# Kernel optimization log

Measured on AMD Instinct MI355X. Metric: run time of the kernel, lower is better.

Reference implementation:

```python
import jax, jax.numpy as jnp
import numpy as np

RES, GATE, SKIP, K, DIL, CIN = 128, 256, 128, 3, 2, 80
PAD = (K - 1) * DIL


def _wn(v, g):
    # weight_norm: w = g * v / ||v||, norm over all dims except dim 0 (out_channels)
    norm = jnp.sqrt(jnp.sum(v * v, axis=(1, 2), keepdims=True))
    return v * (g.reshape(-1, 1, 1) / norm)


def setup_inputs() -> dict:
    key = jax.random.key(0)
    ks = jax.random.split(key, 12)
    s = lambda *sh: 1.0 / np.sqrt(np.prod(sh[1:]))
    d = {
        "x": jax.random.normal(ks[0], (8, RES, 32768), dtype=jnp.float32),
        "condition": jax.random.normal(ks[1], (8, CIN, 32768), dtype=jnp.float32),
        "conv_v": jax.random.normal(ks[2], (GATE, RES, K), dtype=jnp.float32) * s(GATE, RES, K),
        "conv_g": jnp.ones((GATE,), dtype=jnp.float32),
        "conv_b": jnp.zeros((GATE,), dtype=jnp.float32),
        "lc_v": jax.random.normal(ks[3], (GATE, CIN, 1), dtype=jnp.float32) * s(GATE, CIN, 1),
        "lc_g": jnp.ones((GATE,), dtype=jnp.float32),
        "skip_v": jax.random.normal(ks[4], (SKIP, GATE // 2, 1), dtype=jnp.float32) * s(SKIP, GATE // 2, 1),
        "skip_g": jnp.ones((SKIP,), dtype=jnp.float32),
        "skip_b": jnp.zeros((SKIP,), dtype=jnp.float32),
        "out_v": jax.random.normal(ks[5], (RES, GATE // 2, 1), dtype=jnp.float32) * s(RES, GATE // 2, 1),
        "out_g": jnp.ones((RES,), dtype=jnp.float32),
        "out_b": jnp.zeros((RES,), dtype=jnp.float32),
    }
    return d


def reference(x, condition, conv_v, conv_g, conv_b, lc_v, lc_g,
              skip_v, skip_g, skip_b, out_v, out_g, out_b):
    residual = x
    w = _wn(conv_v, conv_g)  # [GATE, RES, K]
    # torch pads symmetrically then slices [:, :, :-PAD]; equivalent to left-only pad
    h = jax.lax.conv_general_dilated(
        x, w, window_strides=(1,), padding=[(PAD, 0)], rhs_dilation=(DIL,),
        dimension_numbers=("NCH", "OIH", "NCH"))
    h = h + conv_b[None, :, None]  # [B, GATE, T]
    a, b = jnp.split(h, 2, axis=1)
    lc_w = _wn(lc_v, lc_g)[:, :, 0]  # [GATE, CIN]
    c = jnp.einsum("oc,bct->bot", lc_w, condition)
    ca, cb = jnp.split(c, 2, axis=1)
    g = jnp.tanh(a + ca) * jax.nn.sigmoid(b + cb)  # [B, GATE//2, T]
    skip_w = _wn(skip_v, skip_g)[:, :, 0]
    s = jnp.einsum("oc,bct->bot", skip_w, g) + skip_b[None, :, None]
    out_w = _wn(out_v, out_g)[:, :, 0]
    o = jnp.einsum("oc,bct->bot", out_w, g) + out_b[None, :, None]
    return (o + residual, s)
```

## Files before the change

kernel.cpp:

```cpp
#include <hip/hip_runtime.h>
#include <hip/hip_bf16.h>

#define B_N   8
#define T_N   32768
#define RESC  128
#define GATEC 256
#define CINC  80
#define CINP  96
#define NT    64
#define HALO  4
#define XROWS 68
#define XSTR  136
#define CSTR  96
#define HSTR  136

#define AP1_ELEMS (16*12*512)
#define AP2_ELEMS (16*3*512)
#define AP3_ELEMS (16*4*512)

#define OFF_S ((size_t)B_N * RESC * T_N)

typedef __attribute__((ext_vector_type(8))) short short8;
typedef __attribute__((ext_vector_type(4))) float f32x4;

__device__ __forceinline__ ushort f2bf(float f) {
  union { float f; unsigned int u; } c; c.f = f;
  unsigned int u = c.u;
  u += 0x7fffu + ((u >> 16) & 1u);
  return (ushort)(u >> 16);
}
__device__ __forceinline__ float bf2f(ushort s) {
  union { unsigned int u; float f; } c; c.u = ((unsigned int)s) << 16;
  return c.f;
}

__global__ __launch_bounds__(256) void wn_pack_kernel(
    const float* __restrict__ conv_v, const float* __restrict__ conv_g,
    const float* __restrict__ lc_v,  const float* __restrict__ lc_g,
    const float* __restrict__ skip_v,const float* __restrict__ skip_g,
    const float* __restrict__ out_v, const float* __restrict__ out_g,
    ushort* __restrict__ Ap1, ushort* __restrict__ Ap2, ushort* __restrict__ Ap3) {
  const int o   = blockIdx.x;
  const int tid = threadIdx.x;
  const int mtg = o >> 4, r = o & 15;
  __shared__ float red[256];

  float s = 0.f;
  for (int e = tid; e < RESC * 3; e += 256) { float v = conv_v[o * RESC * 3 + e]; s += v * v; }
  red[tid] = s; __syncthreads();
  for (int off = 128; off > 0; off >>= 1) { if (tid < off) red[tid] += red[tid + off]; __syncthreads(); }
  const float csc = conv_g[o] / sqrtf(red[0]);
  __syncthreads();
  for (int e = tid; e < 384; e += 256) {
    const int ks = e >> 5, q = (e >> 3) & 3, j = e & 7;
    const int tap = ks >> 2, ci = (ks & 3) * 32 + q * 8 + j;
    Ap1[((mtg * 12 + ks) * 64 + q * 16 + r) * 8 + j] = f2bf(conv_v[(o * RESC + ci) * 3 + tap] * csc);
  }

  s = 0.f;
  for (int e = tid; e < CINC; e += 256) { float v = lc_v[o * CINC + e]; s += v * v; }
  red[tid] = s; __syncthreads();
  for (int off = 128; off > 0; off >>= 1) { if (tid < off) red[tid] += red[tid + off]; __syncthreads(); }
  const float lsc = lc_g[o] / sqrtf(red[0]);
  __syncthreads();
  for (int e = tid; e < CINP; e += 256) {
    const int ks = e >> 5, q = (e >> 3) & 3, j = e & 7;
    const float wv = (e < CINC) ? lc_v[o * CINC + e] * lsc : 0.f;
    Ap2[((mtg * 3 + ks) * 64 + q * 16 + r) * 8 + j] = f2bf(wv);
  }

  const float* vrow = (o < 128) ? (skip_v + o * 128) : (out_v + (o - 128) * 128);
  const float  gg   = (o < 128) ? skip_g[o] : out_g[o - 128];
  s = 0.f;
  for (int e = tid; e < 128; e += 256) { float v = vrow[e]; s += v * v; }
  red[tid] = s; __syncthreads();
  for (int off = 128; off > 0; off >>= 1) { if (tid < off) red[tid] += red[tid + off]; __syncthreads(); }
  const float ssc = gg / sqrtf(red[0]);
  for (int e = tid; e < 128; e += 256) {
    const int ks = e >> 5, q = (e >> 3) & 3, j = e & 7;
    Ap3[((mtg * 4 + ks) * 64 + q * 16 + r) * 8 + j] = f2bf(vrow[e] * ssc);
  }
}

__global__ __launch_bounds__(256) void fused_block_kernel(
    const float* __restrict__ x, const float* __restrict__ cond,
    const float* __restrict__ conv_b, const float* __restrict__ skip_b,
    const float* __restrict__ out_b,
    const ushort* __restrict__ Ap1, const ushort* __restrict__ Ap2,
    const ushort* __restrict__ Ap3,
    float* __restrict__ out) {
  const int tid  = threadIdx.x;
  const int w    = tid >> 6;
  const int lane = tid & 63;
  const int q    = lane >> 4;
  const int n    = lane & 15;
  const int blk  = blockIdx.x;
  const int b    = blk >> 9;
  const int t0   = (blk & 511) << 6;

  __shared__ ushort smem[17408];
  ushort* xs  = smem;
  ushort* cs  = smem + XROWS * XSTR;
  ushort* hsA = smem;
  ushort* hsB = smem + NT * HSTR;

  {
    const int g4 = tid >> 3;
    const int c0 = g4 << 2;
    const int tt = (tid & 7) << 3;
    const float* xp = x + ((size_t)b * RESC + c0) * T_N + t0 + tt;
    float va[4][8];
#pragma unroll
    for (int rr = 0; rr < 4; ++rr) {
      const float4* rp = (const float4*)(xp + (size_t)rr * T_N);
      const float4 a0 = rp[0], a1 = rp[1];
      va[rr][0] = a0.x; va[rr][1] = a0.y; va[rr][2] = a0.z; va[rr][3] = a0.w;
      va[rr][4] = a1.x; va[rr][5] = a1.y; va[rr][6] = a1.z; va[rr][7] = a1.w;
    }
#pragma unroll
    for (int ss = 0; ss < 8; ++ss) {
      const unsigned lo = (unsigned)f2bf(va[0][ss]) | ((unsigned)f2bf(va[1][ss]) << 16);
      const unsigned hi = (unsigned)f2bf(va[2][ss]) | ((unsigned)f2bf(va[3][ss]) << 16);
      *(uint2*)&xs[(HALO + tt + ss) * XSTR + c0] = make_uint2(lo, hi);
    }
  }
  if (tid < RESC) {
    float h0 = 0.f, h1 = 0.f, h2 = 0.f, h3 = 0.f;
    if (t0 > 0) {
      const float4 hv = *(const float4*)(x + ((size_t)b * RESC + tid) * T_N + t0 - 4);
      h0 = hv.x; h1 = hv.y; h2 = hv.z; h3 = hv.w;
    }
    xs[0 * XSTR + tid] = f2bf(h0);
    xs[1 * XSTR + tid] = f2bf(h1);
    xs[2 * XSTR + tid] = f2bf(h2);
    xs[3 * XSTR + tid] = f2bf(h3);
  }
  if (tid < 160) {
    const int g4 = tid >> 3;
    const int c0 = g4 << 2;
    const int tt = (tid & 7) << 3;
    const float* cp = cond + ((size_t)b * CINC + c0) * T_N + t0 + tt;
    float va[4][8];
#pragma unroll
    for (int rr = 0; rr < 4; ++rr) {
      const float4* rp = (const float4*)(cp + (size_t)rr * T_N);
      const float4 a0 = rp[0], a1 = rp[1];
      va[rr][0] = a0.x; va[rr][1] = a0.y; va[rr][2] = a0.z; va[rr][3] = a0.w;
      va[rr][4] = a1.x; va[rr][5] = a1.y; va[rr][6] = a1.z; va[rr][7] = a1.w;
    }
#pragma unroll
    for (int ss = 0; ss < 8; ++ss) {
      const unsigned lo = (unsigned)f2bf(va[0][ss]) | ((unsigned)f2bf(va[1][ss]) << 16);
      const unsigned hi = (unsigned)f2bf(va[2][ss]) | ((unsigned)f2bf(va[3][ss]) << 16);
      *(uint2*)&cs[(tt + ss) * CSTR + c0] = make_uint2(lo, hi);
    }
  } else {
    const int e0 = tid - 160;
    for (int z = e0; z < 512; z += 96) {
      const int t = z >> 3, cp2 = z & 7;
      *(unsigned int*)&cs[t * CSTR + CINC + cp2 * 2] = 0u;
    }
  }
  __syncthreads();

  f32x4 acc[4][4];
#pragma unroll
  for (int mt = 0; mt < 4; ++mt) {
    const float4 cb = *(const float4*)(conv_b + w * 64 + mt * 16 + q * 4);
#pragma unroll
    for (int nt = 0; nt < 4; ++nt) acc[mt][nt] = (f32x4){cb.x, cb.y, cb.z, cb.w};
  }
#pragma unroll
  for (int ks = 0; ks < 12; ++ks) {
    const int tap = ks >> 2;
    const int cb2 = (ks & 3) << 5;
    short8 af[4], bfr[4];
#pragma unroll
    for (int mt = 0; mt < 4; ++mt)
      af[mt] = *(const short8*)(Ap1 + ((w * 4 + mt) * 12 + ks) * 512 + lane * 8);
#pragma unroll
    for (int nt = 0; nt < 4; ++nt)
      bfr[nt] = *(const short8*)&xs[(nt * 16 + n + tap * 2) * XSTR + cb2 + q * 8];
#pragma unroll
    for (int mt = 0; mt < 4; ++mt)
#pragma unroll
      for (int nt = 0; nt < 4; ++nt)
        acc[mt][nt] = __builtin_amdgcn_mfma_f32_16x16x32_bf16(af[mt], bfr[nt], acc[mt][nt], 0, 0, 0);
  }
#pragma unroll
  for (int ks = 0; ks < 3; ++ks) {
    short8 af[4], bfr[4];
#pragma unroll
    for (int mt = 0; mt < 4; ++mt)
      af[mt] = *(const short8*)(Ap2 + ((w * 4 + mt) * 3 + ks) * 512 + lane * 8);
#pragma unroll
    for (int nt = 0; nt < 4; ++nt)
      bfr[nt] = *(const short8*)&cs[(nt * 16 + n) * CSTR + ks * 32 + q * 8];
#pragma unroll
    for (int mt = 0; mt < 4; ++mt)
#pragma unroll
      for (int nt = 0; nt < 4; ++nt)
        acc[mt][nt] = __builtin_amdgcn_mfma_f32_16x16x32_bf16(af[mt], bfr[nt], acc[mt][nt], 0, 0, 0);
  }
  __syncthreads();

  const int colbase = (w & 1) << 6;
  {
    ushort* hdst = (w < 2) ? hsA : hsB;
#pragma unroll
    for (int mt = 0; mt < 4; ++mt)
#pragma unroll
      for (int nt = 0; nt < 4; ++nt) {
        const f32x4 v = acc[mt][nt];
        float r0, r1, r2, r3;
        if (w < 2) {
          r0 = 1.f - 2.f / (__expf(2.f * v[0]) + 1.f);
          r1 = 1.f - 2.f / (__expf(2.f * v[1]) + 1.f);
          r2 = 1.f - 2.f / (__expf(2.f * v[2]) + 1.f);
          r3 = 1.f - 2.f / (__expf(2.f * v[3]) + 1.f);
        } else {
          r0 = 1.f / (1.f + __expf(-v[0]));
          r1 = 1.f / (1.f + __expf(-v[1]));
          r2 = 1.f / (1.f + __expf(-v[2]));
          r3 = 1.f / (1.f + __expf(-v[3]));
        }
        const unsigned lo = (unsigned)f2bf(r0) | ((unsigned)f2bf(r1) << 16);
        const unsigned hi = (unsigned)f2bf(r2) | ((unsigned)f2bf(r3) << 16);
        *(uint2*)&hdst[(nt * 16 + n) * HSTR + colbase + mt * 16 + q * 4] = make_uint2(lo, hi);
      }
  }
  __syncthreads();

  {
    const int prow = tid >> 2;
    const int pc0  = (tid & 3) << 5;
#pragma unroll
    for (int s2 = 0; s2 < 8; ++s2) {
      const int col = pc0 + (s2 << 2);
      const uint2 ua = *(uint2*)&hsA[prow * HSTR + col];
      const uint2 ub = *(uint2*)&hsB[prow * HSTR + col];
      const float a0 = bf2f((ushort)ua.x), a1 = bf2f((ushort)(ua.x >> 16));
      const float a2 = bf2f((ushort)ua.y), a3 = bf2f((ushort)(ua.y >> 16));
      const float b0 = bf2f((ushort)ub.x), b1 = bf2f((ushort)(ub.x >> 16));
      const float b2 = bf2f((ushort)ub.y), b3 = bf2f((ushort)(ub.y >> 16));
      const unsigned lo = (unsigned)f2bf(a0 * b0) | ((unsigned)f2bf(a1 * b1) << 16);
      const unsigned hi = (unsigned)f2bf(a2 * b2) | ((unsigned)f2bf(a3 * b3) << 16);
      *(uint2*)&hsA[prow * HSTR + col] = make_uint2(lo, hi);
    }
  }
  __syncthreads();

  {
    const float* bias = (w < 2) ? skip_b : out_b;
#pragma unroll
    for (int mt = 0; mt < 4; ++mt) {
      const float4 bb = *(const float4*)(bias + colbase + mt * 16 + q * 4);
#pragma unroll
      for (int nt = 0; nt < 4; ++nt) acc[mt][nt] = (f32x4){bb.x, bb.y, bb.z, bb.w};
    }
#pragma unroll
    for (int ks = 0; ks < 4; ++ks) {
      short8 af[4], bfr[4];
#pragma unroll
      for (int mt = 0; mt < 4; ++mt)
        af[mt] = *(const short8*)(Ap3 + ((w * 4 + mt) * 4 + ks) * 512 + lane * 8);
#pragma unroll
      for (int nt = 0; nt < 4; ++nt)
        bfr[nt] = *(const short8*)&hsA[(nt * 16 + n) * HSTR + ks * 32 + q * 8];
#pragma unroll
      for (int mt = 0; mt < 4; ++mt)
#pragma unroll
        for (int nt = 0; nt < 4; ++nt)
          acc[mt][nt] = __builtin_amdgcn_mfma_f32_16x16x32_bf16(af[mt], bfr[nt], acc[mt][nt], 0, 0, 0);
    }
  }

#pragma unroll
  for (int mt = 0; mt < 4; ++mt)
#pragma unroll
    for (int nt = 0; nt < 4; ++nt) {
      const int ch = colbase + mt * 16 + q * 4;
      const int t  = t0 + nt * 16 + n;
      const f32x4 v = acc[mt][nt];
      if (w < 2) {
        float* dst = out + OFF_S + ((size_t)(b * RESC + ch)) * T_N + t;
#pragma unroll
        for (int i = 0; i < 4; ++i) dst[(size_t)i * T_N] = v[i];
      } else {
        const float* xr = x + ((size_t)(b * RESC + ch)) * T_N + t;
        float* dst = out + ((size_t)(b * RESC + ch)) * T_N + t;
#pragma unroll
        for (int i = 0; i < 4; ++i) dst[(size_t)i * T_N] = v[i] + xr[(size_t)i * T_N];
      }
    }
}

extern "C" void kernel_launch(void* const* d_in, const int* in_sizes, int n_in,
                              void* d_out, int out_size, void* d_ws, size_t ws_size,
                              hipStream_t stream) {
  const float* x      = (const float*)d_in[0];
  const float* cond   = (const float*)d_in[1];
  const float* conv_v = (const float*)d_in[2];
  const float* conv_g = (const float*)d_in[3];
  const float* conv_b = (const float*)d_in[4];
  const float* lc_v   = (const float*)d_in[5];
  const float* lc_g   = (const float*)d_in[6];
  const float* skip_v = (const float*)d_in[7];
  const float* skip_g = (const float*)d_in[8];
  const float* skip_b = (const float*)d_in[9];
  const float* out_v  = (const float*)d_in[10];
  const float* out_g  = (const float*)d_in[11];
  const float* out_b  = (const float*)d_in[12];

  ushort* Ap1 = (ushort*)d_ws;
  ushort* Ap2 = Ap1 + AP1_ELEMS;
  ushort* Ap3 = Ap2 + AP2_ELEMS;

  hipLaunchKernelGGL(wn_pack_kernel, dim3(256), dim3(256), 0, stream,
                     conv_v, conv_g, lc_v, lc_g, skip_v, skip_g, out_v, out_g,
                     Ap1, Ap2, Ap3);
  hipLaunchKernelGGL(fused_block_kernel, dim3(4096), dim3(256), 0, stream,
                     x, cond, conv_b, skip_b, out_b, Ap1, Ap2, Ap3, (float*)d_out);
}
```

Baseline: 511.5 us.

## Fuse gating in registers by pairing tanh/sigmoid tiles per wave, swizzle LDS

Each wave now owns matching tanh and sigmoid output tiles (rows 2w,2w+1 and 8+2w,9+2w). The gate product can then be computed in registers, which removes the separate LDS round trip, one bf16 rounding step and one barrier. LDS rows use an XOR swizzle in place of padded strides, and the LDS footprint shrinks. A launch-bounds occupancy hint of 5 blocks per CU is added, which may constrain registers and cause spills.

New measurement: 965.5 us. 1.89x slower.

```diff
diff --git a/kernel.cpp b/kernel.cpp
--- a/kernel.cpp
+++ b/kernel.cpp
@@ -1,5 +1,4 @@
 #include <hip/hip_runtime.h>
-#include <hip/hip_bf16.h>
 
 #define B_N   8
 #define T_N   32768
@@ -10,9 +9,11 @@
 #define NT    64
 #define HALO  4
 #define XROWS 68
-#define XSTR  136
-#define CSTR  96
-#define HSTR  136
+
+#define XSTR_B 272
+#define CSTR_B 208
+#define CS_OFF 18496
+#define LDS_BYTES (18496 + 13312)
 
 #define AP1_ELEMS (16*12*512)
 #define AP2_ELEMS (16*3*512)
@@ -29,9 +30,11 @@
   u += 0x7fffu + ((u >> 16) & 1u);
   return (ushort)(u >> 16);
 }
-__device__ __forceinline__ float bf2f(ushort s) {
-  union { unsigned int u; float f; } c; c.u = ((unsigned int)s) << 16;
-  return c.f;
+
+__device__ __forceinline__ char* lds_at(char* base, int row, int strB, int colB) {
+  int off = row * strB + colB;
+  off ^= ((row >> 3) & 7) << 4;
+  return base + off;
 }
 
 __global__ __launch_bounds__(256) void wn_pack_kernel(
@@ -82,7 +85,7 @@
   }
 }
 
-__global__ __launch_bounds__(256) void fused_block_kernel(
+__global__ __launch_bounds__(256, 5) void fused_block_kernel(
     const float* __restrict__ x, const float* __restrict__ cond,
     const float* __restrict__ conv_b, const float* __restrict__ skip_b,
     const float* __restrict__ out_b,
@@ -98,11 +101,10 @@
   const int b    = blk >> 9;
   const int t0   = (blk & 511) << 6;
 
-  __shared__ ushort smem[17408];
-  ushort* xs  = smem;
-  ushort* cs  = smem + XROWS * XSTR;
-  ushort* hsA = smem;
-  ushort* hsB = smem + NT * HSTR;
+  __shared__ __align__(128) char smem[LDS_BYTES];
+  char* xs = smem;
+  char* cs = smem + CS_OFF;
+  char* gs = smem;
 
   {
     const int g4 = tid >> 3;
@@ -121,7 +123,7 @@
     for (int ss = 0; ss < 8; ++ss) {
       const unsigned lo = (unsigned)f2bf(va[0][ss]) | ((unsigned)f2bf(va[1][ss]) << 16);
       const unsigned hi = (unsigned)f2bf(va[2][ss]) | ((unsigned)f2bf(va[3][ss]) << 16);
-      *(uint2*)&xs[(HALO + tt + ss) * XSTR + c0] = make_uint2(lo, hi);
+      *(uint2*)lds_at(xs, HALO + tt + ss, XSTR_B, c0 * 2) = make_uint2(lo, hi);
     }
   }
   if (tid < RESC) {
@@ -130,10 +132,10 @@
       const float4 hv = *(const float4*)(x + ((size_t)b * RESC + tid) * T_N + t0 - 4);
       h0 = hv.x; h1 = hv.y; h2 = hv.z; h3 = hv.w;
     }
-    xs[0 * XSTR + tid] = f2bf(h0);
-    xs[1 * XSTR + tid] = f2bf(h1);
-    xs[2 * XSTR + tid] = f2bf(h2);
-    xs[3 * XSTR + tid] = f2bf(h3);
+    *(ushort*)lds_at(xs, 0, XSTR_B, tid * 2) = f2bf(h0);
+    *(ushort*)lds_at(xs, 1, XSTR_B, tid * 2) = f2bf(h1);
+    *(ushort*)lds_at(xs, 2, XSTR_B, tid * 2) = f2bf(h2);
+    *(ushort*)lds_at(xs, 3, XSTR_B, tid * 2) = f2bf(h3);
   }
   if (tid < 160) {
     const int g4 = tid >> 3;
@@ -152,35 +154,36 @@
     for (int ss = 0; ss < 8; ++ss) {
       const unsigned lo = (unsigned)f2bf(va[0][ss]) | ((unsigned)f2bf(va[1][ss]) << 16);
       const unsigned hi = (unsigned)f2bf(va[2][ss]) | ((unsigned)f2bf(va[3][ss]) << 16);
-      *(uint2*)&cs[(tt + ss) * CSTR + c0] = make_uint2(lo, hi);
+      *(uint2*)lds_at(cs, tt + ss, CSTR_B, c0 * 2) = make_uint2(lo, hi);
     }
   } else {
     const int e0 = tid - 160;
     for (int z = e0; z < 512; z += 96) {
-      const int t = z >> 3, cp2 = z & 7;
-      *(unsigned int*)&cs[t * CSTR + CINC + cp2 * 2] = 0u;
-    }
-  }
-  __syncthreads();
-
+      const int row = z >> 3, c = z & 7;
+      *(unsigned int*)lds_at(cs, row, CSTR_B, 160 + c * 4) = 0u;
+    }
+  }
+  __syncthreads();
+
+  const int mtile[4] = {2 * w, 2 * w + 1, 8 + 2 * w, 9 + 2 * w};
   f32x4 acc[4][4];
 #pragma unroll
   for (int mt = 0; mt < 4; ++mt) {
-    const float4 cb = *(const float4*)(conv_b + w * 64 + mt * 16 + q * 4);
+    const float4 cb = *(const float4*)(conv_b + mtile[mt] * 16 + q * 4);
 #pragma unroll
     for (int nt = 0; nt < 4; ++nt) acc[mt][nt] = (f32x4){cb.x, cb.y, cb.z, cb.w};
   }
 #pragma unroll
   for (int ks = 0; ks < 12; ++ks) {
     const int tap = ks >> 2;
-    const int cb2 = (ks & 3) << 5;
+    const int cbyte = ((ks & 3) << 6);
     short8 af[4], bfr[4];
 #pragma unroll
     for (int mt = 0; mt < 4; ++mt)
-      af[mt] = *(const short8*)(Ap1 + ((w * 4 + mt) * 12 + ks) * 512 + lane * 8);
+      af[mt] = *(const short8*)(Ap1 + ((mtile[mt] * 12 + ks) * 64 + lane) * 8);
 #pragma unroll
     for (int nt = 0; nt < 4; ++nt)
-      bfr[nt] = *(const short8*)&xs[(nt * 16 + n + tap * 2) * XSTR + cb2 + q * 8];
+      bfr[nt] = *(const short8*)lds_at(xs, nt * 16 + n + tap * 2, XSTR_B, cbyte + q * 16);
 #pragma unroll
     for (int mt = 0; mt < 4; ++mt)
 #pragma unroll
@@ -192,10 +195,10 @@
     short8 af[4], bfr[4];
 #pragma unroll
     for (int mt = 0; mt < 4; ++mt)
-      af[mt] = *(const short8*)(Ap2 + ((w * 4 + mt) * 3 + ks) * 512 + lane * 8);
+      af[mt] = *(const short8*)(Ap2 + ((mtile[mt] * 3 + ks) * 64 + lane) * 8);
 #pragma unroll
     for (int nt = 0; nt < 4; ++nt)
-      bfr[nt] = *(const short8*)&cs[(nt * 16 + n) * CSTR + ks * 32 + q * 8];
+      bfr[nt] = *(const short8*)lds_at(cs, nt * 16 + n, CSTR_B, ks * 64 + q * 16);
 #pragma unroll
     for (int mt = 0; mt < 4; ++mt)
 #pragma unroll
@@ -204,53 +207,27 @@
   }
   __syncthreads();
 
+#pragma unroll
+  for (int mt = 0; mt < 2; ++mt)
+#pragma unroll
+    for (int nt = 0; nt < 4; ++nt) {
+      const f32x4 va = acc[mt][nt];
+      const f32x4 vb = acc[mt + 2][nt];
+      float r[4];
+#pragma unroll
+      for (int i = 0; i < 4; ++i) {
+        const float ta = 1.f - 2.f / (__expf(2.f * va[i]) + 1.f);
+        const float sb = 1.f / (1.f + __expf(-vb[i]));
+        r[i] = ta * sb;
+      }
+      const unsigned lo = (unsigned)f2bf(r[0]) | ((unsigned)f2bf(r[1]) << 16);
+      const unsigned hi = (unsigned)f2bf(r[2]) | ((unsigned)f2bf(r[3]) << 16);
+      *(uint2*)lds_at(gs, nt * 16 + n, XSTR_B, 64 * w + 32 * mt + 8 * q) = make_uint2(lo, hi);
+    }
+  __syncthreads();
+
   const int colbase = (w & 1) << 6;
   {
-    ushort* hdst = (w < 2) ? hsA : hsB;
-#pragma unroll
-    for (int mt = 0; mt < 4; ++mt)
-#pragma unroll
-      for (int nt = 0; nt < 4; ++nt) {
-        const f32x4 v = acc[mt][nt];
-        float r0, r1, r2, r3;
-        if (w < 2) {
-          r0 = 1.f - 2.f / (__expf(2.f * v[0]) + 1.f);
-          r1 = 1.f - 2.f / (__expf(2.f * v[1]) + 1.f);
-          r2 = 1.f - 2.f / (__expf(2.f * v[2]) + 1.f);
-          r3 = 1.f - 2.f / (__expf(2.f * v[3]) + 1.f);
-        } else {
-          r0 = 1.f / (1.f + __expf(-v[0]));
-          r1 = 1.f / (1.f + __expf(-v[1]));
-          r2 = 1.f / (1.f + __expf(-v[2]));
-          r3 = 1.f / (1.f + __expf(-v[3]));
-        }
-        const unsigned lo = (unsigned)f2bf(r0) | ((unsigned)f2bf(r1) << 16);
-        const unsigned hi = (unsigned)f2bf(r2) | ((unsigned)f2bf(r3) << 16);
-        *(uint2*)&hdst[(nt * 16 + n) * HSTR + colbase + mt * 16 + q * 4] = make_uint2(lo, hi);
-      }
-  }
-  __syncthreads();
-
-  {
-    const int prow = tid >> 2;
-    const int pc0  = (tid & 3) << 5;
-#pragma unroll
-    for (int s2 = 0; s2 < 8; ++s2) {
-      const int col = pc0 + (s2 << 2);
-      const uint2 ua = *(uint2*)&hsA[prow * HSTR + col];
-      const uint2 ub = *(uint2*)&hsB[prow * HSTR + col];
-      const float a0 = bf2f((ushort)ua.x), a1 = bf2f((ushort)(ua.x >> 16));
-      const float a2 = bf2f((ushort)ua.y), a3 = bf2f((ushort)(ua.y >> 16));
-      const float b0 = bf2f((ushort)ub.x), b1 = bf2f((ushort)(ub.x >> 16));
-      const float b2 = bf2f((ushort)ub.y), b3 = bf2f((ushort)(ub.y >> 16));
-      const unsigned lo = (unsigned)f2bf(a0 * b0) | ((unsigned)f2bf(a1 * b1) << 16);
-      const unsigned hi = (unsigned)f2bf(a2 * b2) | ((unsigned)f2bf(a3 * b3) << 16);
-      *(uint2*)&hsA[prow * HSTR + col] = make_uint2(lo, hi);
-    }
-  }
-  __syncthreads();
-
-  {
     const float* bias = (w < 2) ? skip_b : out_b;
 #pragma unroll
     for (int mt = 0; mt < 4; ++mt) {
@@ -266,7 +243,7 @@
         af[mt] = *(const short8*)(Ap3 + ((w * 4 + mt) * 4 + ks) * 512 + lane * 8);
 #pragma unroll
       for (int nt = 0; nt < 4; ++nt)
-        bfr[nt] = *(const short8*)&hsA[(nt * 16 + n) * HSTR + ks * 32 + q * 8];
+        bfr[nt] = *(const short8*)lds_at(gs, nt * 16 + n, XSTR_B, ks * 64 + q * 16);
 #pragma unroll
       for (int mt = 0; mt < 4; ++mt)
 #pragma unroll
```
